# Optimization experiments

Hardware: AMD Instinct MI355X
Metric: run time of the kernel (lower is better)

The kernel has to match this reference:

```python
import jax, jax.numpy as jnp
import numpy as np
from jax import lax

D_MODEL = 1024
D_STATE = 16
D_CONV = 4
EXPAND = 2
D_INNER = D_MODEL * EXPAND
B, T = 2, 1024


def setup_inputs() -> dict:
    key = jax.random.key(0)
    ks = jax.random.split(key, 8)
    s = 0.02
    x = jax.random.normal(ks[0], (B, T, D_MODEL), dtype=jnp.float32)
    in_proj_w = jax.random.normal(ks[1], (D_MODEL, 2 * D_INNER), dtype=jnp.float32) * s
    conv_w = jax.random.normal(ks[2], (D_INNER, 1, D_CONV), dtype=jnp.float32) * s  # depthwise [O, I/G=1, K]
    conv_b = jax.random.normal(ks[3], (D_INNER,), dtype=jnp.float32) * s
    x_proj_w = jax.random.normal(ks[4], (D_INNER, 2 * D_STATE + 1), dtype=jnp.float32) * s
    dt_proj_w = jax.random.normal(ks[5], (1, D_INNER), dtype=jnp.float32) * s
    dt_proj_b = jax.random.normal(ks[6], (D_INNER,), dtype=jnp.float32) * s
    # Canonical Mamba init: A_log = log(1..d_state) broadcast over d_inner
    A_log = jnp.broadcast_to(jnp.log(jnp.arange(1, D_STATE + 1, dtype=jnp.float32))[None, :], (D_INNER, D_STATE))
    D_param = jnp.ones((D_INNER,), dtype=jnp.float32)
    c_proj_w = jax.random.normal(ks[7], (D_INNER, D_MODEL), dtype=jnp.float32) * s
    return {"x": x, "in_proj_w": in_proj_w, "conv_w": conv_w, "conv_b": conv_b,
            "x_proj_w": x_proj_w, "dt_proj_w": dt_proj_w, "dt_proj_b": dt_proj_b,
            "A_log": A_log, "D_param": D_param, "c_proj_w": c_proj_w}


def _mamba_fwd(x, in_proj_w, conv_w, conv_b, x_proj_w, dt_proj_w, dt_proj_b, A_log, D_param, c_proj_w):
    Bb, Tt, _ = x.shape
    xz = jnp.einsum('btd,de->bte', x, in_proj_w)          # [B,T,2*Di]
    x_branch, z = jnp.split(xz, 2, axis=-1)               # [B,T,Di] each
    # Causal depthwise conv1d: pad left K-1 (== torch pad both + slice[:T])
    xb = jnp.transpose(x_branch, (0, 2, 1))               # [B,Di,T]
    xb = lax.conv_general_dilated(xb, conv_w, window_strides=(1,),
                                  padding=[(D_CONV - 1, 0)],
                                  feature_group_count=D_INNER,
                                  dimension_numbers=('NCH', 'OIH', 'NCH'))
    xb = xb + conv_b[None, :, None]
    x_branch = jax.nn.silu(jnp.transpose(xb, (0, 2, 1)))  # [B,T,Di]
    x_ssm = jnp.einsum('btd,dk->btk', x_branch, x_proj_w) # [B,T,2S+1]
    B_t = x_ssm[:, :, :D_STATE]                            # [B,T,S]
    C_t = x_ssm[:, :, D_STATE:2 * D_STATE]                 # [B,T,S]
    dt = x_ssm[:, :, -1:]                                  # [B,T,1]
    dt = jax.nn.softplus(jnp.einsum('btk,kd->btd', dt, dt_proj_w) + dt_proj_b)  # [B,T,Di]
    A = -jnp.exp(A_log)                                    # [Di,S]
    A_bar = jnp.exp(dt[..., None] * A[None, None])         # [B,T,Di,S]
    Bx = (dt[..., None] * B_t[:, :, None, :]) * x_branch[..., None]  # [B,T,Di,S]

    def step(h, inp):
        a, bx, c = inp                                     # [B,Di,S],[B,Di,S],[B,S]
        h = a * h + bx
        y = jnp.einsum('bds,bs->bd', h, c)
        return h, y

    h0 = jnp.zeros((Bb, D_INNER, D_STATE), dtype=x.dtype)
    _, ys = lax.scan(step, h0,
                     (jnp.transpose(A_bar, (1, 0, 2, 3)),
                      jnp.transpose(Bx, (1, 0, 2, 3)),
                      jnp.transpose(C_t, (1, 0, 2))))
    y = jnp.transpose(ys, (1, 0, 2))                       # [B,T,Di]
    y = y + D_param[None, None, :] * x_branch
    y = y * jax.nn.silu(z)
    return jnp.einsum('btd,de->bte', y, c_proj_w)          # [B,T,d_model]


def reference(x, in_proj_w, conv_w, conv_b, x_proj_w, dt_proj_w, dt_proj_b, A_log, D_param, c_proj_w):
    return _mamba_fwd(x, in_proj_w, conv_w, conv_b, x_proj_w, dt_proj_w, dt_proj_b, A_log, D_param, c_proj_w)
```

## Files before the change

kernel.cpp:

```cpp
#include <hip/hip_runtime.h>
#include <math.h>

#define DMODEL 1024
#define DSTATE 16
#define DCONV 4
#define DINNER 2048
#define BATCH 2
#define SEQ 1024
#define BT (BATCH*SEQ)
#define NC 32
#define LC 32

typedef unsigned short ushort_t;
typedef __attribute__((ext_vector_type(8))) short short8;
typedef __attribute__((ext_vector_type(4))) float f32x4;

__device__ __forceinline__ ushort_t f2bf(float f) {
    union { float f; unsigned int u; } v; v.f = f;
    unsigned int r = v.u + 0x7fffu + ((v.u >> 16) & 1u);
    return (ushort_t)(r >> 16);
}
__device__ __forceinline__ float bf2f(ushort_t u) {
    union { unsigned int u; float f; } v; v.u = ((unsigned int)u) << 16;
    return v.f;
}
__device__ __forceinline__ float softplusf(float x) {
    return (x > 20.f) ? x : log1pf(__expf(x));
}

#define GLOAD_LDS16(G, L) \
  __builtin_amdgcn_global_load_lds((const __attribute__((address_space(1))) void*)(G), \
                                   (__attribute__((address_space(3))) void*)(L), 16, 0, 0)

__global__ __launch_bounds__(256) void prep_kernel(const float* __restrict__ x,
                                                   ushort_t* __restrict__ xbf,
                                                   const float* __restrict__ w1,
                                                   ushort_t* __restrict__ w1T,
                                                   const float* __restrict__ w2,
                                                   ushort_t* __restrict__ w2T,
                                                   const float* __restrict__ wx,
                                                   ushort_t* __restrict__ wT,
                                                   float* __restrict__ zacc)
{
    __shared__ float t[32][33];
    const int bid = blockIdx.x;
    const int tid = threadIdx.x;

    if (bid < 1024) {
        size_t i = ((size_t)bid * 256 + tid) * 8;
        float4 a = *(const float4*)&x[i];
        float4 b = *(const float4*)&x[i + 4];
        uint4 p;
        p.x = (unsigned)f2bf(a.x) | ((unsigned)f2bf(a.y) << 16);
        p.y = (unsigned)f2bf(a.z) | ((unsigned)f2bf(a.w) << 16);
        p.z = (unsigned)f2bf(b.x) | ((unsigned)f2bf(b.y) << 16);
        p.w = (unsigned)f2bf(b.z) | ((unsigned)f2bf(b.w) << 16);
        *(uint4*)&xbf[i] = p;
        if (bid < 66) {
            size_t z = ((size_t)bid * 256 + tid) * 4;
            *(float4*)&zacc[z] = make_float4(0.f, 0.f, 0.f, 0.f);
        }
        return;
    }

    if (bid >= 7168) {
        __shared__ ushort_t th[32][48];
        __shared__ ushort_t tl[32][48];
        const int r0 = (bid - 7168) * 32;
        for (int e = tid; e < 32 * 48; e += 256) {
            int k = e / 48, n = e % 48;
            float v = (n < 33) ? wx[(size_t)(r0 + k) * 33 + n] : 0.f;
            ushort_t hi = f2bf(v);
            th[k][n] = hi;
            tl[k][n] = f2bf(v - bf2f(hi));
        }
        __syncthreads();
        for (int e = tid; e < 48 * 32; e += 256) {
            int n = e >> 5, k = e & 31;
            wT[(size_t)n * DINNER + r0 + k]        = th[k][n];
            wT[(size_t)(48 + n) * DINNER + r0 + k] = tl[k][n];
        }
        return;
    }

    const float* in; ushort_t* out; int R, Cc, r0, c0;
    if (bid < 5120) {
        int b2 = bid - 1024;
        in = w1; out = w1T; R = DMODEL; Cc = 2 * DINNER;
        r0 = (b2 >> 7) * 32; c0 = (b2 & 127) * 32;
    } else {
        int b3 = bid - 5120;
        in = w2; out = w2T; R = DINNER; Cc = DMODEL;
        r0 = (b3 >> 5) * 32; c0 = (b3 & 31) * 32;
    }
    {
        int lr = tid >> 3, lc4 = (tid & 7) * 4;
        float4 v = *(const float4*)&in[(size_t)(r0 + lr) * Cc + c0 + lc4];
        t[lr][lc4 + 0] = v.x; t[lr][lc4 + 1] = v.y;
        t[lr][lc4 + 2] = v.z; t[lr][lc4 + 3] = v.w;
    }
    __syncthreads();
    {
        int oc = tid >> 3, rq = (tid & 7) * 4;
        ushort4 u;
        u.x = f2bf(t[rq + 0][oc]);
        u.y = f2bf(t[rq + 1][oc]);
        u.z = f2bf(t[rq + 2][oc]);
        u.w = f2bf(t[rq + 3][oc]);
        *(ushort4*)&out[(size_t)(c0 + oc) * R + r0 + rq] = u;
    }
}

__global__ __launch_bounds__(256) void gemm_in(const ushort_t* __restrict__ A,
                                               const ushort_t* __restrict__ Bt,
                                               float* __restrict__ xzx,
                                               ushort_t* __restrict__ zsil)
{
    constexpr int BM = 128, BN = 128, BK = 64;
    constexpr int AL = BM * BK / (256 * 8);
    constexpr int BL = BN * BK / (256 * 8);
    constexpr int FM = BM / 32;
    constexpr int FN = BN / 32;
    const int K = DMODEL;
    __shared__ __align__(16) ushort_t Al[BM * BK];
    __shared__ __align__(16) ushort_t Bl[BN * BK];

    const int tid  = threadIdx.x;
    const int lane = tid & 63;
    const int wid  = tid >> 6;
    const int wr   = wid >> 1;
    const int wc   = wid & 1;
    const int bm   = blockIdx.y * BM;
    const int bn   = blockIdx.x * BN;

    f32x4 acc[FM][FN] = {};

    for (int k0 = 0; k0 < K; k0 += BK) {
#pragma unroll
        for (int j = 0; j < AL; j++) {
            int chunk = j * 256 + tid;
            GLOAD_LDS16(&A[(size_t)(bm + (chunk >> 3)) * K + k0 + (chunk & 7) * 8],
                        &Al[(size_t)(j * 256 + wid * 64) * 8]);
        }
#pragma unroll
        for (int j = 0; j < BL; j++) {
            int chunk = j * 256 + tid;
            GLOAD_LDS16(&Bt[(size_t)(bn + (chunk >> 3)) * K + k0 + (chunk & 7) * 8],
                        &Bl[(size_t)(j * 256 + wid * 64) * 8]);
        }
        __syncthreads();

#pragma unroll
        for (int kk = 0; kk < 2; kk++) {
            short8 af[FM], bf[FN];
#pragma unroll
            for (int m = 0; m < FM; m++)
                af[m] = *(const short8*)&Al[(wr * (BM / 2) + m * 16 + (lane & 15)) * BK
                                            + (lane >> 4) * 8 + kk * 32];
#pragma unroll
            for (int n = 0; n < FN; n++)
                bf[n] = *(const short8*)&Bl[(wc * (BN / 2) + n * 16 + (lane & 15)) * BK
                                            + (lane >> 4) * 8 + kk * 32];
#pragma unroll
            for (int m = 0; m < FM; m++)
#pragma unroll
                for (int n = 0; n < FN; n++)
                    acc[m][n] = __builtin_amdgcn_mfma_f32_16x16x32_bf16(af[m], bf[n], acc[m][n], 0, 0, 0);
        }
        __syncthreads();
    }

    if (bn < DINNER) {
#pragma unroll
        for (int m = 0; m < FM; m++)
#pragma unroll
            for (int n = 0; n < FN; n++) {
                int row0 = bm + wr * (BM / 2) + m * 16 + (lane >> 4) * 4;
                int col  = bn + wc * (BN / 2) + n * 16 + (lane & 15);
#pragma unroll
                for (int r = 0; r < 4; r++)
                    xzx[(size_t)(row0 + r) * DINNER + col] = acc[m][n][r];
            }
    } else {
#pragma unroll
        for (int m = 0; m < FM; m++)
#pragma unroll
            for (int n = 0; n < FN; n++) {
                int row0 = bm + wr * (BM / 2) + m * 16 + (lane >> 4) * 4;
                int col  = bn - DINNER + wc * (BN / 2) + n * 16 + (lane & 15);
#pragma unroll
                for (int r = 0; r < 4; r++) {
                    float z = acc[m][n][r];
                    zsil[(size_t)(row0 + r) * DINNER + col] = f2bf(z / (1.f + __expf(-z)));
                }
            }
    }
}

template<int BM, int BN>
__global__ __launch_bounds__(256) void gemm_bt(const ushort_t* __restrict__ A,
                                               const ushort_t* __restrict__ Bt,
                                               float* __restrict__ C,
                                               int M, int N, int K)
{
    constexpr int BK = 64;
    constexpr int AL = BM * BK / (256 * 8);
    constexpr int BL = BN * BK / (256 * 8);
    constexpr int FM = BM / 32;
    constexpr int FN = BN / 32;
    __shared__ __align__(16) ushort_t Al[BM * BK];
    __shared__ __align__(16) ushort_t Bl[BN * BK];

    const int tid  = threadIdx.x;
    const int lane = tid & 63;
    const int wid  = tid >> 6;
    const int wr   = wid >> 1;
    const int wc   = wid & 1;
    const int bm   = blockIdx.y * BM;
    const int bn   = blockIdx.x * BN;

    f32x4 acc[FM][FN] = {};

    for (int k0 = 0; k0 < K; k0 += BK) {
#pragma unroll
        for (int j = 0; j < AL; j++) {
            int chunk = j * 256 + tid;
            GLOAD_LDS16(&A[(size_t)(bm + (chunk >> 3)) * K + k0 + (chunk & 7) * 8],
                        &Al[(size_t)(j * 256 + wid * 64) * 8]);
        }
#pragma unroll
        for (int j = 0; j < BL; j++) {
            int chunk = j * 256 + tid;
            GLOAD_LDS16(&Bt[(size_t)(bn + (chunk >> 3)) * K + k0 + (chunk & 7) * 8],
                        &Bl[(size_t)(j * 256 + wid * 64) * 8]);
        }
        __syncthreads();

#pragma unroll
        for (int kk = 0; kk < 2; kk++) {
            short8 af[FM], bf[FN];
#pragma unroll
            for (int m = 0; m < FM; m++)
                af[m] = *(const short8*)&Al[(wr * (BM / 2) + m * 16 + (lane & 15)) * BK
                                            + (lane >> 4) * 8 + kk * 32];
#pragma unroll
            for (int n = 0; n < FN; n++)
                bf[n] = *(const short8*)&Bl[(wc * (BN / 2) + n * 16 + (lane & 15)) * BK
                                            + (lane >> 4) * 8 + kk * 32];
#pragma unroll
            for (int m = 0; m < FM; m++)
#pragma unroll
                for (int n = 0; n < FN; n++)
                    acc[m][n] = __builtin_amdgcn_mfma_f32_16x16x32_bf16(af[m], bf[n], acc[m][n], 0, 0, 0);
        }
        __syncthreads();
    }

#pragma unroll
    for (int m = 0; m < FM; m++)
#pragma unroll
        for (int n = 0; n < FN; n++) {
            int row0 = bm + wr * (BM / 2) + m * 16 + (lane >> 4) * 4;
            int col  = bn + wc * (BN / 2) + n * 16 + (lane & 15);
#pragma unroll
            for (int r = 0; r < 4; r++)
                C[(size_t)(row0 + r) * N + col] = acc[m][n][r];
        }
}

__global__ __launch_bounds__(256) void xproj_mfma(const ushort_t* __restrict__ A,
                                                  const ushort_t* __restrict__ wT,
                                                  float* __restrict__ Btb,
                                                  float* __restrict__ Ctb,
                                                  float* __restrict__ dtraw)
{
    constexpr int BK = 64;
    __shared__ __align__(16) ushort_t Al[64 * BK];
    __shared__ __align__(16) ushort_t Bl[96 * BK];

    const int tid  = threadIdx.x;
    const int lane = tid & 63;
    const int wid  = tid >> 6;
    const int kc   = blockIdx.x * 256;
    const int bm   = blockIdx.y * 64;

    f32x4 acc[6] = {};

    for (int ks = 0; ks < 4; ks++) {
        const int kbase = kc + ks * BK;
#pragma unroll
        for (int j = 0; j < 2; j++) {
            int chunk = j * 256 + tid;
            GLOAD_LDS16(&A[(size_t)(bm + (chunk >> 3)) * DINNER + kbase + (chunk & 7) * 8],
                        &Al[(size_t)(j * 256 + wid * 64) * 8]);
        }
#pragma unroll
        for (int j = 0; j < 3; j++) {
            int chunk = j * 256 + tid;
            GLOAD_LDS16(&wT[(size_t)(chunk >> 3) * DINNER + kbase + (chunk & 7) * 8],
                        &Bl[(size_t)(j * 256 + wid * 64) * 8]);
        }
        __syncthreads();

#pragma unroll
        for (int kk = 0; kk < 2; kk++) {
            short8 af = *(const short8*)&Al[(wid * 16 + (lane & 15)) * BK
                                            + (lane >> 4) * 8 + kk * 32];
#pragma unroll
            for (int n = 0; n < 6; n++) {
                short8 bf = *(const short8*)&Bl[(n * 16 + (lane & 15)) * BK
                                                + (lane >> 4) * 8 + kk * 32];
                acc[n] = __builtin_amdgcn_mfma_f32_16x16x32_bf16(af, bf, acc[n], 0, 0, 0);
            }
        }
        __syncthreads();
    }

    const int n   = lane & 15;
    const int row = bm + wid * 16 + (lane >> 4) * 4;
#pragma unroll
    for (int nf = 0; nf < 3; nf++) {
        f32x4 v = acc[nf] + acc[nf + 3];
        int ng = nf * 16 + n;
        if (ng < 16) {
#pragma unroll
            for (int r = 0; r < 4; r++)
                atomicAdd(&Btb[(size_t)(row + r) * 16 + ng], v[r]);
        } else if (ng < 32) {
#pragma unroll
            for (int r = 0; r < 4; r++)
                atomicAdd(&Ctb[(size_t)(row + r) * 16 + (ng - 16)], v[r]);
        } else if (ng == 32) {
#pragma unroll
            for (int r = 0; r < 4; r++)
                atomicAdd(&dtraw[row + r], v[r]);
        }
    }
}

__global__ __launch_bounds__(256) void conv_silu_kernel(const float* __restrict__ xzx,
                                                        const float* __restrict__ cw,
                                                        const float* __restrict__ cb,
                                                        ushort_t* __restrict__ xbb)
{
    __shared__ float tile[64 + 3][64];
    const int b  = blockIdx.z;
    const int t0 = blockIdx.x * 64;
    const int d0 = blockIdx.y * 64;
    const int tid = threadIdx.x;

    for (int e = tid; e < 67 * 16; e += 256) {
        int r  = e / 16;
        int c4 = (e % 16) * 4;
        int t  = t0 - 3 + r;
        float4 v = make_float4(0.f, 0.f, 0.f, 0.f);
        if (t >= 0)
            v = *(const float4*)&xzx[((size_t)b * SEQ + t) * DINNER + d0 + c4];
        *(float4*)&tile[r][c4] = v;
    }
    __syncthreads();

    const int dl = tid & 63;
    const int tb = tid >> 6;
    const int d  = d0 + dl;
    const float w0 = cw[d * 4 + 0], w1 = cw[d * 4 + 1];
    const float w2 = cw[d * 4 + 2], w3 = cw[d * 4 + 3];
    const float bias = cb[d];

#pragma unroll
    for (int ii = 0; ii < 16; ii++) {
        int tl = tb + 4 * ii;
        float s = bias;
        s = fmaf(tile[tl + 0][dl], w0, s);
        s = fmaf(tile[tl + 1][dl], w1, s);
        s = fmaf(tile[tl + 2][dl], w2, s);
        s = fmaf(tile[tl + 3][dl], w3, s);
        float sil = s / (1.f + __expf(-s));
        xbb[((size_t)b * SEQ + t0 + tl) * DINNER + d] = f2bf(sil);
    }
}

__device__ __forceinline__ void qpowers(float q, float* a)
{
    float q2 = q * q, q4 = q2 * q2, q8 = q4 * q4;
    a[0] = q;        a[1] = q2;       a[2] = q2 * q;   a[3] = q4;
    a[4] = q4 * q;   a[5] = q4 * q2;  a[6] = q4 * a[2];a[7] = q8;
    a[8] = q8 * q;   a[9] = q8 * q2;  a[10]= q8 * a[2];a[11]= q8 * q4;
    a[12]= q8 * a[4];a[13]= q8 * a[5];a[14]= q8 * a[6];a[15]= q8 * q8;
}

__device__ __forceinline__ bool a_structure_ok(const float* A_log, int d, float As2_0)
{
    bool ok = true;
#pragma unroll
    for (int s = 1; s < 16; s++) {
        float v = -__expf(A_log[d * 16 + s]) * 1.44269504f;
        ok &= (fabsf(v - (float)(s + 1) * As2_0) <= 1e-4f * (float)(s + 1) * fabsf(As2_0));
    }
    return ok;
}

__device__ __forceinline__ void stage_xs(const ushort_t* __restrict__ xbb,
                                         float (*xs)[256],
                                         int b, int t0, int d0, int tid)
{
#pragma unroll
    for (int j = 0; j < 4; j++) {
        int e = j * 256 + tid;
        int rr = e >> 5, cc8 = (e & 31) * 8;
        short8 v = *(const short8*)&xbb[((size_t)b * SEQ + t0 + rr) * DINNER + d0 + cc8];
#pragma unroll
        for (int k = 0; k < 8; k++)
            xs[rr][cc8 + k] = bf2f((ushort_t)v[k]);
    }
}

__global__ __launch_bounds__(256) void scan1_kernel(const ushort_t* __restrict__ xbb,
                                                    const float* __restrict__ dtraw,
                                                    const float* __restrict__ Btb,
                                                    const float* __restrict__ A_log,
                                                    const float* __restrict__ dtw,
                                                    const float* __restrict__ dtb,
                                                    float* __restrict__ Hend,
                                                    float* __restrict__ dtsum)
{
    __shared__ float raw[LC];
    __shared__ float xs[LC][256];
    __shared__ float Bs[LC][16];

    const int tid = threadIdx.x;
    const int c   = blockIdx.x;
    const int b   = blockIdx.z;
    const int d0  = blockIdx.y * 256;
    const int d   = d0 + tid;
    const int t0  = c * LC;

    if (tid < LC / 4)
        *(float4*)&raw[tid * 4] = *(const float4*)&dtraw[b * SEQ + t0 + tid * 4];
    if (tid < 128)
        *(float4*)&Bs[0][tid * 4] = *(const float4*)&Btb[((size_t)b * SEQ + t0) * 16 + tid * 4];
    stage_xs(xbb, xs, b, t0, d0, tid);

    const float wd = dtw[d], bd = dtb[d];
    const float As2_0 = -__expf(A_log[d * 16]) * 1.44269504f;
    const bool fast = a_structure_ok(A_log, d, As2_0);

    float h[16];
#pragma unroll
    for (int s = 0; s < 16; s++) h[s] = 0.f;
    float dsum = 0.f;
    __syncthreads();

    if (fast) {
#pragma unroll 2
        for (int t = 0; t < LC; t++) {
            float dt = softplusf(fmaf(raw[t], wd, bd));
            float xv = xs[t][tid];
            float Bv[16];
#pragma unroll
            for (int s4 = 0; s4 < 4; s4++)
                *(float4*)&Bv[s4 * 4] = *(const float4*)&Bs[t][s4 * 4];
            float a[16];
            qpowers(exp2f(dt * As2_0), a);
            float dtx = dt * xv;
            dsum += dt;
#pragma unroll
            for (int s = 0; s < 16; s++)
                h[s] = fmaf(a[s], h[s], Bv[s] * dtx);
        }
    } else {
        float As2[16];
#pragma unroll
        for (int s = 0; s < 16; s++)
            As2[s] = -__expf(A_log[d * 16 + s]) * 1.44269504f;
#pragma unroll 2
        for (int t = 0; t < LC; t++) {
            float dt = softplusf(fmaf(raw[t], wd, bd));
            float xv = xs[t][tid];
            float Bv[16];
#pragma unroll
            for (int s4 = 0; s4 < 4; s4++)
                *(float4*)&Bv[s4 * 4] = *(const float4*)&Bs[t][s4 * 4];
            float dtx = dt * xv;
            dsum += dt;
#pragma unroll
            for (int s = 0; s < 16; s++)
                h[s] = fmaf(exp2f(dt * As2[s]), h[s], Bv[s] * dtx);
        }
    }

    size_t hb = (((size_t)b * NC + c) * DINNER + d) * 16;
#pragma unroll
    for (int s4 = 0; s4 < 4; s4++)
        *(float4*)&Hend[hb + s4 * 4] = *(float4*)&h[s4 * 4];
    dtsum[((size_t)b * NC + c) * DINNER + d] = dsum;
}

__global__ __launch_bounds__(256) void carry_kernel(const float* __restrict__ Hend,
                                                    const float* __restrict__ dtsum,
                                                    const float* __restrict__ A_log,
                                                    float* __restrict__ Hstart)
{
    const int idx = blockIdx.x * 256 + threadIdx.x;
    const int s = idx & 15;
    const int d = (idx >> 4) & (DINNER - 1);
    const int b = idx >> 15;
    const float As2 = -__expf(A_log[d * 16 + s]) * 1.44269504f;
    float hs = 0.f;
    for (int c = 0; c < NC; c++) {
        size_t off = ((size_t)b * NC + c);
        float P  = exp2f(As2 * dtsum[off * DINNER + d]);
        size_t hi = (off * DINNER + d) * 16 + s;
        float he = Hend[hi];
        Hstart[hi] = hs;
        hs = fmaf(P, hs, he);
    }
}

__global__ __launch_bounds__(256) void scan3_kernel(const ushort_t* __restrict__ xbb,
                                                    const float* __restrict__ dtraw,
                                                    const float* __restrict__ Btb,
                                                    const float* __restrict__ Ctb,
                                                    const float* __restrict__ A_log,
                                                    const float* __restrict__ dtw,
                                                    const float* __restrict__ dtb,
                                                    const float* __restrict__ Hstart,
                                                    const ushort_t* __restrict__ zsil,
                                                    const float* __restrict__ Dp,
                                                    ushort_t* __restrict__ ygb)
{
    __shared__ float raw[LC];
    __shared__ float xs[LC][256];
    __shared__ float Bs[LC][16];
    __shared__ float Cs[LC][16];

    const int tid = threadIdx.x;
    const int c   = blockIdx.x;
    const int b   = blockIdx.z;
    const int d0  = blockIdx.y * 256;
    const int d   = d0 + tid;
    const int t0  = c * LC;

    if (tid < LC / 4)
        *(float4*)&raw[tid * 4] = *(const float4*)&dtraw[b * SEQ + t0 + tid * 4];
    if (tid < 128)
        *(float4*)&Bs[0][tid * 4] = *(const float4*)&Btb[((size_t)b * SEQ + t0) * 16 + tid * 4];
    else {
        int u = tid - 128;
        *(float4*)&Cs[0][u * 4] = *(const float4*)&Ctb[((size_t)b * SEQ + t0) * 16 + u * 4];
    }
    stage_xs(xbb, xs, b, t0, d0, tid);

    const float wd = dtw[d], bd = dtb[d];
    const float Dd = Dp[d];
    const float As2_0 = -__expf(A_log[d * 16]) * 1.44269504f;
    const bool fast = a_structure_ok(A_log, d, As2_0);

    float h[16];
    {
        size_t hb = (((size_t)b * NC + c) * DINNER + d) * 16;
#pragma unroll
        for (int s4 = 0; s4 < 4; s4++)
            *(float4*)&h[s4 * 4] = *(const float4*)&Hstart[hb + s4 * 4];
    }
    __syncthreads();

    if (fast) {
#pragma unroll 2
        for (int t = 0; t < LC; t++) {
            float dt = softplusf(fmaf(raw[t], wd, bd));
            float xv = xs[t][tid];
            float Bv[16], Cv[16];
#pragma unroll
            for (int s4 = 0; s4 < 4; s4++) {
                *(float4*)&Bv[s4 * 4] = *(const float4*)&Bs[t][s4 * 4];
                *(float4*)&Cv[s4 * 4] = *(const float4*)&Cs[t][s4 * 4];
            }
            float a[16];
            qpowers(exp2f(dt * As2_0), a);
            float dtx = dt * xv;
            float acc = 0.f;
#pragma unroll
            for (int s = 0; s < 16; s++) {
                h[s] = fmaf(a[s], h[s], Bv[s] * dtx);
                acc = fmaf(h[s], Cv[s], acc);
            }
            xs[t][tid] = fmaf(Dd, xv, acc);
        }
    } else {
        float As2[16];
#pragma unroll
        for (int s = 0; s < 16; s++)
            As2[s] = -__expf(A_log[d * 16 + s]) * 1.44269504f;
#pragma unroll 2
        for (int t = 0; t < LC; t++) {
            float dt = softplusf(fmaf(raw[t], wd, bd));
            float xv = xs[t][tid];
            float Bv[16], Cv[16];
#pragma unroll
            for (int s4 = 0; s4 < 4; s4++) {
                *(float4*)&Bv[s4 * 4] = *(const float4*)&Bs[t][s4 * 4];
                *(float4*)&Cv[s4 * 4] = *(const float4*)&Cs[t][s4 * 4];
            }
            float dtx = dt * xv;
            float acc = 0.f;
#pragma unroll
            for (int s = 0; s < 16; s++) {
                h[s] = fmaf(exp2f(dt * As2[s]), h[s], Bv[s] * dtx);
                acc = fmaf(h[s], Cv[s], acc);
            }
            xs[t][tid] = fmaf(Dd, xv, acc);
        }
    }
    __syncthreads();

#pragma unroll
    for (int j = 0; j < 8; j++) {
        int e = j * 256 + tid;
        int rr = e >> 6, c4 = (e & 63) * 4;
        float4 yv = *(const float4*)&xs[rr][c4];
        ushort4 zv = *(const ushort4*)&zsil[((size_t)b * SEQ + t0 + rr) * DINNER + d0 + c4];
        ushort4 u;
        u.x = f2bf(yv.x * bf2f(zv.x));
        u.y = f2bf(yv.y * bf2f(zv.y));
        u.z = f2bf(yv.z * bf2f(zv.z));
        u.w = f2bf(yv.w * bf2f(zv.w));
        *(ushort4*)&ygb[((size_t)b * SEQ + t0 + rr) * DINNER + d0 + c4] = u;
    }
}

extern "C" void kernel_launch(void* const* d_in, const int* in_sizes, int n_in,
                              void* d_out, int out_size, void* d_ws, size_t ws_size,
                              hipStream_t stream)
{
    const float* x         = (const float*)d_in[0];
    const float* in_proj_w = (const float*)d_in[1];
    const float* conv_w    = (const float*)d_in[2];
    const float* conv_b    = (const float*)d_in[3];
    const float* x_proj_w  = (const float*)d_in[4];
    const float* dt_proj_w = (const float*)d_in[5];
    const float* dt_proj_b = (const float*)d_in[6];
    const float* A_log     = (const float*)d_in[7];
    const float* D_param   = (const float*)d_in[8];
    const float* c_proj_w  = (const float*)d_in[9];
    float* out = (float*)d_out;

    float* ws    = (float*)d_ws;
    float* xzx   = ws;
    float* Btb   = xzx + (size_t)BT * DINNER;
    float* Ctb   = Btb + (size_t)BT * 16;
    float* dtraw = Ctb + (size_t)BT * 16;
    float* Hend  = dtraw + BT;
    float* Hstart= Hend + (size_t)BATCH * NC * DINNER * 16;
    float* dtsum = Hstart + (size_t)BATCH * NC * DINNER * 16;
    ushort_t* xbf  = (ushort_t*)(dtsum + (size_t)BATCH * NC * DINNER);
    ushort_t* w1T  = xbf + (size_t)BT * DMODEL;
    ushort_t* w2T  = w1T + (size_t)(2 * DINNER) * DMODEL;
    ushort_t* ygb  = w2T + (size_t)DMODEL * DINNER;
    ushort_t* zsil = ygb + (size_t)BT * DINNER;
    ushort_t* xbb  = zsil + (size_t)BT * DINNER;
    ushort_t* wT   = xbb + (size_t)BT * DINNER;

    prep_kernel<<<dim3(1024 + 4096 + 2048 + 64), 256, 0, stream>>>(
        x, xbf, in_proj_w, w1T, c_proj_w, w2T, x_proj_w, wT, Btb);

    gemm_in<<<dim3((2 * DINNER) / 128, BT / 128), 256, 0, stream>>>(
        xbf, w1T, xzx, zsil);

    conv_silu_kernel<<<dim3(SEQ / 64, DINNER / 64, BATCH), 256, 0, stream>>>(
        xzx, conv_w, conv_b, xbb);

    xproj_mfma<<<dim3(8, 32), 256, 0, stream>>>(xbb, wT, Btb, Ctb, dtraw);

    scan1_kernel<<<dim3(NC, DINNER / 256, BATCH), 256, 0, stream>>>(
        xbb, dtraw, Btb, A_log, dt_proj_w, dt_proj_b, Hend, dtsum);
    carry_kernel<<<dim3(BATCH * DINNER * 16 / 256), 256, 0, stream>>>(
        Hend, dtsum, A_log, Hstart);
    scan3_kernel<<<dim3(NC, DINNER / 256, BATCH), 256, 0, stream>>>(
        xbb, dtraw, Btb, Ctb, A_log, dt_proj_w, dt_proj_b, Hstart, zsil, D_param, ygb);

    gemm_bt<64, 64><<<dim3(DMODEL / 64, BT / 64), 256, 0, stream>>>(
        ygb, w2T, out, BT, DMODEL, DINNER);
}
```

Measured before the change: 143.0 us.

## Store x-branch projection as bf16 and add XCD-aware block swizzle to GEMMs

The in-projection GEMM now writes the x branch as bf16 instead of fp32, and the conv kernel reads bf16 vectors and widens them. This halves the write and reread traffic of the 2048x2048 intermediate. Both GEMMs also remap the linear block index so that consecutive tiles land on the same XCD, which should improve L2 reuse across the chiplets. The cost is an extra rounding of the pre-conv activations to bf16, which adds precision loss.

```diff
diff --git a/kernel.cpp b/kernel.cpp
--- a/kernel.cpp
+++ b/kernel.cpp
@@ -31,6 +31,10 @@
 #define GLOAD_LDS16(G, L) \
   __builtin_amdgcn_global_load_lds((const __attribute__((address_space(1))) void*)(G), \
                                    (__attribute__((address_space(3))) void*)(L), 16, 0, 0)
+
+__device__ __forceinline__ int xcd_swz512(int lin) {
+    return (lin & 7) * 64 + (lin >> 3);
+}
 
 __global__ __launch_bounds__(256) void prep_kernel(const float* __restrict__ x,
                                                    ushort_t* __restrict__ xbf,
@@ -113,7 +117,7 @@
 
 __global__ __launch_bounds__(256) void gemm_in(const ushort_t* __restrict__ A,
                                                const ushort_t* __restrict__ Bt,
-                                               float* __restrict__ xzx,
+                                               ushort_t* __restrict__ xzb,
                                                ushort_t* __restrict__ zsil)
 {
     constexpr int BM = 128, BN = 128, BK = 64;
@@ -130,8 +134,9 @@
     const int wid  = tid >> 6;
     const int wr   = wid >> 1;
     const int wc   = wid & 1;
-    const int bm   = blockIdx.y * BM;
-    const int bn   = blockIdx.x * BN;
+    const int swz  = xcd_swz512(blockIdx.y * 32 + blockIdx.x);
+    const int bm   = (swz >> 5) * BM;
+    const int bn   = (swz & 31) * BN;
 
     f32x4 acc[FM][FN] = {};
 
@@ -179,7 +184,7 @@
                 int col  = bn + wc * (BN / 2) + n * 16 + (lane & 15);
 #pragma unroll
                 for (int r = 0; r < 4; r++)
-                    xzx[(size_t)(row0 + r) * DINNER + col] = acc[m][n][r];
+                    xzb[(size_t)(row0 + r) * DINNER + col] = f2bf(acc[m][n][r]);
             }
     } else {
 #pragma unroll
@@ -197,17 +202,16 @@
     }
 }
 
-template<int BM, int BN>
-__global__ __launch_bounds__(256) void gemm_bt(const ushort_t* __restrict__ A,
-                                               const ushort_t* __restrict__ Bt,
-                                               float* __restrict__ C,
-                                               int M, int N, int K)
-{
-    constexpr int BK = 64;
+__global__ __launch_bounds__(256) void gemm_out(const ushort_t* __restrict__ A,
+                                                const ushort_t* __restrict__ Bt,
+                                                float* __restrict__ C)
+{
+    constexpr int BM = 64, BN = 64, BK = 64;
     constexpr int AL = BM * BK / (256 * 8);
     constexpr int BL = BN * BK / (256 * 8);
     constexpr int FM = BM / 32;
     constexpr int FN = BN / 32;
+    const int M = BT, N = DMODEL, K = DINNER;
     __shared__ __align__(16) ushort_t Al[BM * BK];
     __shared__ __align__(16) ushort_t Bl[BN * BK];
 
@@ -216,8 +220,9 @@
     const int wid  = tid >> 6;
     const int wr   = wid >> 1;
     const int wc   = wid & 1;
-    const int bm   = blockIdx.y * BM;
-    const int bn   = blockIdx.x * BN;
+    const int swz  = xcd_swz512(blockIdx.y * 16 + blockIdx.x);
+    const int bm   = (swz >> 4) * BM;
+    const int bn   = (swz & 15) * BN;
 
     f32x4 acc[FM][FN] = {};
 
@@ -338,7 +343,7 @@
     }
 }
 
-__global__ __launch_bounds__(256) void conv_silu_kernel(const float* __restrict__ xzx,
+__global__ __launch_bounds__(256) void conv_silu_kernel(const ushort_t* __restrict__ xzb,
                                                         const float* __restrict__ cw,
                                                         const float* __restrict__ cb,
                                                         ushort_t* __restrict__ xbb)
@@ -349,14 +354,20 @@
     const int d0 = blockIdx.y * 64;
     const int tid = threadIdx.x;
 
-    for (int e = tid; e < 67 * 16; e += 256) {
-        int r  = e / 16;
-        int c4 = (e % 16) * 4;
+    for (int e = tid; e < 67 * 8; e += 256) {
+        int r  = e >> 3;
+        int c8 = (e & 7) * 8;
         int t  = t0 - 3 + r;
-        float4 v = make_float4(0.f, 0.f, 0.f, 0.f);
-        if (t >= 0)
-            v = *(const float4*)&xzx[((size_t)b * SEQ + t) * DINNER + d0 + c4];
-        *(float4*)&tile[r][c4] = v;
+        if (t >= 0) {
+            short8 v = *(const short8*)&xzb[((size_t)b * SEQ + t) * DINNER + d0 + c8];
+#pragma unroll
+            for (int k = 0; k < 8; k++)
+                tile[r][c8 + k] = bf2f((ushort_t)v[k]);
+        } else {
+#pragma unroll
+            for (int k = 0; k < 8; k++)
+                tile[r][c8 + k] = 0.f;
+        }
     }
     __syncthreads();
 
@@ -646,8 +657,7 @@
     float* out = (float*)d_out;
 
     float* ws    = (float*)d_ws;
-    float* xzx   = ws;
-    float* Btb   = xzx + (size_t)BT * DINNER;
+    float* Btb   = ws;
     float* Ctb   = Btb + (size_t)BT * 16;
     float* dtraw = Ctb + (size_t)BT * 16;
     float* Hend  = dtraw + BT;
@@ -659,16 +669,16 @@
     ushort_t* ygb  = w2T + (size_t)DMODEL * DINNER;
     ushort_t* zsil = ygb + (size_t)BT * DINNER;
     ushort_t* xbb  = zsil + (size_t)BT * DINNER;
-    ushort_t* wT   = xbb + (size_t)BT * DINNER;
+    ushort_t* xzb  = xbb + (size_t)BT * DINNER;
+    ushort_t* wT   = xzb + (size_t)BT * DINNER;
 
     prep_kernel<<<dim3(1024 + 4096 + 2048 + 64), 256, 0, stream>>>(
         x, xbf, in_proj_w, w1T, c_proj_w, w2T, x_proj_w, wT, Btb);
 
-    gemm_in<<<dim3((2 * DINNER) / 128, BT / 128), 256, 0, stream>>>(
-        xbf, w1T, xzx, zsil);
+    gemm_in<<<dim3(32, 16), 256, 0, stream>>>(xbf, w1T, xzb, zsil);
 
     conv_silu_kernel<<<dim3(SEQ / 64, DINNER / 64, BATCH), 256, 0, stream>>>(
-        xzx, conv_w, conv_b, xbb);
+        xzb, conv_w, conv_b, xbb);
 
     xproj_mfma<<<dim3(8, 32), 256, 0, stream>>>(xbb, wT, Btb, Ctb, dtraw);
 
@@ -679,6 +689,5 @@
     scan3_kernel<<<dim3(NC, DINNER / 256, BATCH), 256, 0, stream>>>(
         xbb, dtraw, Btb, Ctb, A_log, dt_proj_w, dt_proj_b, Hstart, zsil, D_param, ygb);
 
-    gemm_bt<64, 64><<<dim3(DMODEL / 64, BT / 64), 256, 0, stream>>>(
-        ygb, w2T, out, BT, DMODEL, DINNER);
-}
+    gemm_out<<<dim3(16, 32), 256, 0, stream>>>(ygb, w2T, out);
+}
```

New measurement: 146.4 us. 2.4% more time.
